# Kernel tuning notes

Measured on AMD Instinct MI355X. Metric: run time of the kernel, lower is better.

## Reference

```python
import jax, jax.numpy as jnp
import numpy as np

B, T, H, E = 256, 256, 512, 96  # batch, enc seq len, hidden/enc dim, charset size


def setup_inputs() -> dict:
    key = jax.random.key(0)
    ks = jax.random.split(key, 9)
    s = 0.05  # param scale
    return {
        "prev_h": jax.random.normal(ks[0], (B, H), jnp.float32),
        "prev_c": jax.random.normal(ks[1], (B, H), jnp.float32),
        "batch_H": jax.random.normal(ks[2], (B, T, H), jnp.float32),
        "char_onehots": jax.nn.one_hot(jax.random.randint(ks[3], (B,), 0, E), E, dtype=jnp.float32),
        "W_i2h": jax.random.normal(ks[4], (H, H), jnp.float32) * s,
        "W_h2h": jax.random.normal(ks[5], (H, H), jnp.float32) * s,
        "b_h2h": jnp.zeros((H,), jnp.float32),
        "w_score": jax.random.normal(ks[6], (H, 1), jnp.float32) * s,
        "W_lstm": jax.random.normal(ks[7], (H + E, 4 * H), jnp.float32) * s,
        "U_lstm": jax.random.normal(ks[8], (H, 4 * H), jnp.float32) * s,
        "b_lstm": jnp.zeros((4 * H,), jnp.float32),
    }


def reference(prev_h, prev_c, batch_H, char_onehots,
              W_i2h, W_h2h, b_h2h, w_score, W_lstm, U_lstm, b_lstm):
    # Additive (Bahdanau) attention
    proj = jnp.einsum('btd,dh->bth', batch_H, W_i2h)          # [B,T,H]
    hp = prev_h @ W_h2h + b_h2h                               # [B,H]
    e = jnp.tanh(proj + hp[:, None, :]) @ w_score             # [B,T,1]
    alpha = jax.nn.softmax(e, axis=1)                         # [B,T,1]
    context = jnp.einsum('bt,btd->bd', alpha[..., 0], batch_H)  # [B,D]
    x = jnp.concatenate([context, char_onehots], axis=1)      # [B,D+E]
    # Keras LSTMCell: gate order i, f, c(g), o
    z = x @ W_lstm + prev_h @ U_lstm + b_lstm                 # [B,4H]
    i, f, g, o = jnp.split(z, 4, axis=1)
    c_new = jax.nn.sigmoid(f) * prev_c + jax.nn.sigmoid(i) * jnp.tanh(g)
    h_new = jax.nn.sigmoid(o) * jnp.tanh(c_new)
    return h_new, c_new, alpha
```

## Files before the change

### kernel.cpp

```cpp
#include <hip/hip_runtime.h>
#include <hip/hip_bf16.h>
#include <math.h>

#define Bq 256
#define Tq 256
#define Hq 512
#define Eq 96

typedef __attribute__((ext_vector_type(8))) short short8;
typedef __attribute__((ext_vector_type(4))) float f32x4;

static __device__ __forceinline__ unsigned short f2bf(float f) {
  union { float f; unsigned u; } v; v.f = f;
  unsigned r = v.u + 0x7FFF + ((v.u >> 16) & 1);
  return (unsigned short)(r >> 16);
}

static __device__ __forceinline__ ushort4 pack4(float4 v) {
  ushort4 p;
  p.x = f2bf(v.x); p.y = f2bf(v.y); p.z = f2bf(v.z); p.w = f2bf(v.w);
  return p;
}

static __device__ __forceinline__ float sat_tanh(float x) {
  float ax = fminf(fabsf(x), 15.0f);
  float e = __builtin_exp2f(ax * 2.885390082f);
  float t = 1.0f - 2.0f / (e + 1.0f);
  return copysignf(t, x);
}

static __device__ __forceinline__ float sat_sig(float x) {
  float cx = fmaxf(fminf(x, 30.0f), -30.0f);
  return 1.0f / (1.0f + __builtin_exp2f(-cx * 1.442695041f));
}

__global__ __launch_bounds__(256) void convW_k(const float* __restrict__ W,
                                               unsigned short* __restrict__ Wt) {
  __shared__ float tile[32][33];
  int bx = blockIdx.x & 15, by = blockIdx.x >> 4;
  int tx = threadIdx.x & 31, ty = threadIdx.x >> 5;
  #pragma unroll
  for (int i = 0; i < 32; i += 8)
    tile[ty + i][tx] = W[(size_t)(by * 32 + ty + i) * Hq + bx * 32 + tx];
  __syncthreads();
  #pragma unroll
  for (int i = 0; i < 32; i += 8)
    Wt[(size_t)(bx * 32 + ty + i) * Hq + by * 32 + tx] = f2bf(tile[tx][ty + i]);
}

__global__ __launch_bounds__(256) void hsplit_k(const float* __restrict__ ph,
                                                const float* __restrict__ Whh,
                                                float* __restrict__ hp) {
  __shared__ __align__(16) float xs[8][128];
  const int ks = blockIdx.x & 3;
  const int nc = (blockIdx.x >> 2) & 3;
  const int bg = blockIdx.x >> 4;
  const int tid = threadIdx.x;
  const int row0 = bg * 8;
  const int d0 = ks * 128;
  for (int i = tid; i < 8 * 32; i += 256) {
    int r = i >> 5, dd = (i & 31) * 4;
    *(float4*)&xs[r][dd] = *(const float4*)&ph[(size_t)(row0 + r) * Hq + d0 + dd];
  }
  __syncthreads();
  const int rt = tid >> 6;
  const int ct = tid & 63;
  const int n = nc * 128 + ct * 2;
  float a00 = 0, a01 = 0, a10 = 0, a11 = 0;
  for (int dd = 0; dd < 128; dd += 4) {
    float4 x0 = *(const float4*)&xs[rt * 2][dd];
    float4 x1 = *(const float4*)&xs[rt * 2 + 1][dd];
    #pragma unroll
    for (int j = 0; j < 4; j++) {
      float2 w = *(const float2*)&Whh[(size_t)(d0 + dd + j) * Hq + n];
      float xj0 = ((const float*)&x0)[j];
      float xj1 = ((const float*)&x1)[j];
      a00 += xj0 * w.x; a01 += xj0 * w.y;
      a10 += xj1 * w.x; a11 += xj1 * w.y;
    }
  }
  int row = row0 + rt * 2;
  atomicAdd(&hp[(size_t)row * Hq + n], a00);
  atomicAdd(&hp[(size_t)row * Hq + n + 1], a01);
  atomicAdd(&hp[(size_t)(row + 1) * Hq + n], a10);
  atomicAdd(&hp[(size_t)(row + 1) * Hq + n + 1], a11);
}

#define LDK 40

__global__ __launch_bounds__(256, 2) void fused_score_k(
    const float* __restrict__ A,
    const unsigned short* __restrict__ Wt,
    const float* __restrict__ hp,
    const float* __restrict__ bh,
    const float* __restrict__ wsc,
    float* __restrict__ e) {
  __shared__ unsigned short As[2][64 * LDK];
  __shared__ float red[4][64];

  const int tid = threadIdx.x;
  const int m0 = blockIdx.x * 64;
  const int b = m0 >> 8;
  const int wave = tid >> 6;
  const int lane = tid & 63;
  const int quad = lane >> 4;
  const int l16 = lane & 15;
  const int wn = wave * 128;

  const int arow = tid >> 3;
  const int acol = (tid & 7) * 4;
  const float* Ab = A + (size_t)m0 * Hq;
  const unsigned short* Bp = Wt + (size_t)(wn + l16) * Hq + quad * 8;

  f32x4 acc[4][8] = {};

  {
    float4 v0 = *(const float4*)&Ab[(size_t)arow * Hq + acol];
    float4 v1 = *(const float4*)&Ab[(size_t)(arow + 32) * Hq + acol];
    *(ushort4*)&As[0][arow * LDK + acol] = pack4(v0);
    *(ushort4*)&As[0][(arow + 32) * LDK + acol] = pack4(v1);
  }
  __syncthreads();

  for (int step = 0; step < 16; step++) {
    const int k0 = step * 32;
    const int cur = step & 1;

    float4 n0v, n1v;
    if (step < 15) {
      n0v = *(const float4*)&Ab[(size_t)arow * Hq + k0 + 32 + acol];
      n1v = *(const float4*)&Ab[(size_t)(arow + 32) * Hq + k0 + 32 + acol];
    }

    short8 bfr[8];
    #pragma unroll
    for (int ni = 0; ni < 8; ni++)
      bfr[ni] = *(const short8*)(Bp + (size_t)ni * 16 * Hq + k0);

    short8 af[4];
    #pragma unroll
    for (int mi = 0; mi < 4; mi++)
      af[mi] = *(const short8*)&As[cur][(mi * 16 + l16) * LDK + quad * 8];

    #pragma unroll
    for (int mi = 0; mi < 4; mi++)
      #pragma unroll
      for (int ni = 0; ni < 8; ni++)
        acc[mi][ni] = __builtin_amdgcn_mfma_f32_16x16x32_bf16(
            af[mi], bfr[ni], acc[mi][ni], 0, 0, 0);

    if (step < 15) {
      *(ushort4*)&As[cur ^ 1][arow * LDK + acol] = pack4(n0v);
      *(ushort4*)&As[cur ^ 1][(arow + 32) * LDK + acol] = pack4(n1v);
    }
    __syncthreads();
  }

  float hv[8], wv[8];
  #pragma unroll
  for (int ni = 0; ni < 8; ni++) {
    int c = wn + ni * 16 + l16;
    hv[ni] = hp[(size_t)b * Hq + c] + bh[c];
    wv[ni] = wsc[c];
  }
  #pragma unroll
  for (int mi = 0; mi < 4; mi++) {
    float s[4] = {0, 0, 0, 0};
    #pragma unroll
    for (int ni = 0; ni < 8; ni++)
      #pragma unroll
      for (int r = 0; r < 4; r++)
        s[r] += sat_tanh(acc[mi][ni][r] + hv[ni]) * wv[ni];
    #pragma unroll
    for (int r = 0; r < 4; r++) {
      s[r] += __shfl_xor(s[r], 8, 64);
      s[r] += __shfl_xor(s[r], 4, 64);
      s[r] += __shfl_xor(s[r], 2, 64);
      s[r] += __shfl_xor(s[r], 1, 64);
    }
    if (l16 == 0) {
      #pragma unroll
      for (int r = 0; r < 4; r++) red[wave][mi * 16 + quad * 4 + r] = s[r];
    }
  }
  __syncthreads();
  if (tid < 64)
    e[m0 + tid] = red[0][tid] + red[1][tid] + red[2][tid] + red[3][tid];
}

__global__ __launch_bounds__(256) void softmax_k(float* __restrict__ ea) {
  __shared__ float red[8];
  int b = blockIdx.x, t = threadIdx.x;
  int wave = t >> 6, lane = t & 63;
  float x = ea[b * Tq + t];
  float m = x;
  #pragma unroll
  for (int off = 32; off >= 1; off >>= 1) m = fmaxf(m, __shfl_xor(m, off, 64));
  if (lane == 0) red[wave] = m;
  __syncthreads();
  m = fmaxf(fmaxf(red[0], red[1]), fmaxf(red[2], red[3]));
  float ex = __builtin_exp2f((x - m) * 1.442695041f);
  float s = ex;
  #pragma unroll
  for (int off = 32; off >= 1; off >>= 1) s += __shfl_xor(s, off, 64);
  if (lane == 0) red[4 + wave] = s;
  __syncthreads();
  s = red[4] + red[5] + red[6] + red[7];
  ea[b * Tq + t] = ex / s;
}

__global__ __launch_bounds__(256) void ctxsplit_k(const float* __restrict__ alpha,
                                                  const float* __restrict__ bH,
                                                  float* __restrict__ ctx) {
  __shared__ float al[64];
  const int b = blockIdx.x >> 2;
  const int tc = blockIdx.x & 3;
  const int tid = threadIdx.x;
  if (tid < 64) al[tid] = alpha[b * Tq + tc * 64 + tid];
  __syncthreads();
  const float2* Hp = (const float2*)(bH + (size_t)b * Tq * Hq + (size_t)tc * 64 * Hq);
  float ax = 0.f, ay = 0.f;
  #pragma unroll 8
  for (int t = 0; t < 64; t++) {
    float a = al[t];
    float2 v = Hp[t * (Hq / 2) + tid];
    ax += a * v.x;
    ay += a * v.y;
  }
  atomicAdd(&ctx[(size_t)b * Hq + 2 * tid], ax);
  atomicAdd(&ctx[(size_t)b * Hq + 2 * tid + 1], ay);
}

__global__ __launch_bounds__(256) void zsplit_k(
    const float* __restrict__ ctx, const float* __restrict__ oneh,
    const float* __restrict__ ph, const float* __restrict__ Wl,
    const float* __restrict__ Ul, float* __restrict__ z) {
  __shared__ __align__(16) float xs[8 * 280];
  const int ks = blockIdx.x & 3;
  const int hc = (blockIdx.x >> 2) & 7;
  const int bg = blockIdx.x >> 5;
  const int tid = threadIdx.x;
  const int row0 = bg * 8;
  const int dbase = ks * 280;

  for (int i = tid; i < 8 * 280; i += 256) {
    int r = i / 280, dd = i % 280;
    int g = dbase + dd;
    float v;
    if (g < 512) v = ctx[(size_t)(row0 + r) * Hq + g];
    else if (g < 608) v = oneh[(row0 + r) * Eq + (g - 512)];
    else v = ph[(size_t)(row0 + r) * Hq + (g - 608)];
    xs[r * 280 + dd] = v;
  }
  __syncthreads();

  const int rt = tid >> 6;
  const int ct = tid & 63;
  const int c0 = ct * 4;
  const int gate = c0 >> 6;
  const int ho = c0 & 63;
  const int n = gate * 512 + hc * 64 + ho;

  float acc0[4] = {0, 0, 0, 0};
  float acc1[4] = {0, 0, 0, 0};
  const float* xr0 = &xs[(rt * 2) * 280];
  const float* xr1 = &xs[(rt * 2 + 1) * 280];

  for (int dd = 0; dd < 280; dd += 4) {
    float4 x0 = *(const float4*)&xr0[dd];
    float4 x1 = *(const float4*)&xr1[dd];
    #pragma unroll
    for (int j = 0; j < 4; j++) {
      int d = dbase + dd + j;
      const float* wp = (d < 608) ? &Wl[(size_t)d * 2048 + n]
                                  : &Ul[(size_t)(d - 608) * 2048 + n];
      float4 w = *(const float4*)wp;
      float a = ((const float*)&x0)[j], b = ((const float*)&x1)[j];
      acc0[0] += a * w.x; acc0[1] += a * w.y; acc0[2] += a * w.z; acc0[3] += a * w.w;
      acc1[0] += b * w.x; acc1[1] += b * w.y; acc1[2] += b * w.z; acc1[3] += b * w.w;
    }
  }
  const int r0 = row0 + rt * 2;
  #pragma unroll
  for (int j = 0; j < 4; j++) {
    atomicAdd(&z[(size_t)r0 * 2048 + n + j], acc0[j]);
    atomicAdd(&z[(size_t)(r0 + 1) * 2048 + n + j], acc1[j]);
  }
}

__global__ __launch_bounds__(256) void gatesz_k(const float* __restrict__ z,
                                                const float* __restrict__ bl,
                                                const float* __restrict__ pc,
                                                float* __restrict__ outh,
                                                float* __restrict__ outc) {
  int p = blockIdx.x * 256 + threadIdx.x;
  #pragma unroll
  for (int q = 0; q < 2; q++, p += 65536) {
    int r = p >> 9, h = p & 511;
    const float* zb = z + (size_t)r * 2048;
    float gi = zb[h] + bl[h];
    float gf = zb[512 + h] + bl[512 + h];
    float gg = zb[1024 + h] + bl[1024 + h];
    float go = zb[1536 + h] + bl[1536 + h];
    float cn = sat_sig(gf) * pc[p] + sat_sig(gi) * sat_tanh(gg);
    float hn = sat_sig(go) * sat_tanh(cn);
    outh[p] = hn;
    outc[p] = cn;
  }
}

#define KXc 1120
__global__ __launch_bounds__(256) void zgates2_k(
    const float* __restrict__ ctx, const float* __restrict__ oneh,
    const float* __restrict__ ph, const float* __restrict__ pc,
    const float* __restrict__ Wl, const float* __restrict__ Ul,
    const float* __restrict__ bl,
    float* __restrict__ outh, float* __restrict__ outc) {
  __shared__ __align__(16) float xs[8 * KXc];
  const int bg = blockIdx.x >> 3;
  const int hc = blockIdx.x & 7;
  const int tid = threadIdx.x;
  const int row0 = bg * 8;

  for (int i = tid; i < 8 * 128; i += 256) {
    int r = i >> 7, dd = (i & 127) * 4;
    *(float4*)&xs[r * KXc + dd] = *(const float4*)&ctx[(size_t)(row0 + r) * Hq + dd];
  }
  for (int i = tid; i < 8 * 128; i += 256) {
    int r = i >> 7, dd = (i & 127) * 4;
    *(float4*)&xs[r * KXc + 608 + dd] = *(const float4*)&ph[(size_t)(row0 + r) * Hq + dd];
  }
  if (tid < 8 * 24) {
    int r = tid / 24, dd = (tid % 24) * 4;
    *(float4*)&xs[r * KXc + 512 + dd] = *(const float4*)&oneh[(row0 + r) * Eq + dd];
  }
  __syncthreads();

  const int rt = tid >> 6;
  const int ct = tid & 63;
  const int c0 = ct * 4;
  const int gate = c0 >> 6;
  const int ho = c0 & 63;
  const int n = gate * 512 + hc * 64 + ho;

  float acc0[4] = {0, 0, 0, 0};
  float acc1[4] = {0, 0, 0, 0};
  const float* xr0 = &xs[(rt * 2) * KXc];
  const float* xr1 = &xs[(rt * 2 + 1) * KXc];

  for (int d = 0; d < 608; d += 4) {
    float4 x0 = *(const float4*)&xr0[d];
    float4 x1 = *(const float4*)&xr1[d];
    #pragma unroll
    for (int j = 0; j < 4; j++) {
      float4 w = *(const float4*)&Wl[(size_t)(d + j) * 2048 + n];
      float a = ((const float*)&x0)[j], b = ((const float*)&x1)[j];
      acc0[0] += a * w.x; acc0[1] += a * w.y; acc0[2] += a * w.z; acc0[3] += a * w.w;
      acc1[0] += b * w.x; acc1[1] += b * w.y; acc1[2] += b * w.z; acc1[3] += b * w.w;
    }
  }
  for (int d = 0; d < 512; d += 4) {
    float4 x0 = *(const float4*)&xr0[608 + d];
    float4 x1 = *(const float4*)&xr1[608 + d];
    #pragma unroll
    for (int j = 0; j < 4; j++) {
      float4 w = *(const float4*)&Ul[(size_t)(d + j) * 2048 + n];
      float a = ((const float*)&x0)[j], b = ((const float*)&x1)[j];
      acc0[0] += a * w.x; acc0[1] += a * w.y; acc0[2] += a * w.z; acc0[3] += a * w.w;
      acc1[0] += b * w.x; acc1[1] += b * w.y; acc1[2] += b * w.z; acc1[3] += b * w.w;
    }
  }

  __syncthreads();
  float* zs = xs;
  #pragma unroll
  for (int j = 0; j < 4; j++) {
    zs[(rt * 2) * 256 + c0 + j] = acc0[j];
    zs[(rt * 2 + 1) * 256 + c0 + j] = acc1[j];
  }
  __syncthreads();

  #pragma unroll
  for (int p = tid; p < 512; p += 256) {
    int r = p >> 6, o = p & 63;
    int h = hc * 64 + o;
    int grow = row0 + r;
    float gi = zs[r * 256 + o]       + bl[h];
    float gf = zs[r * 256 + 64 + o]  + bl[512 + h];
    float gg = zs[r * 256 + 128 + o] + bl[1024 + h];
    float go = zs[r * 256 + 192 + o] + bl[1536 + h];
    float cn = sat_sig(gf) * pc[(size_t)grow * Hq + h] + sat_sig(gi) * sat_tanh(gg);
    float hn = sat_sig(go) * sat_tanh(cn);
    outh[(size_t)grow * Hq + h] = hn;
    outc[(size_t)grow * Hq + h] = cn;
  }
}

extern "C" void kernel_launch(void* const* d_in, const int* in_sizes, int n_in,
                              void* d_out, int out_size, void* d_ws, size_t ws_size,
                              hipStream_t stream) {
  const float* prev_h = (const float*)d_in[0];
  const float* prev_c = (const float*)d_in[1];
  const float* batch_H = (const float*)d_in[2];
  const float* oneh = (const float*)d_in[3];
  const float* W_i2h = (const float*)d_in[4];
  const float* W_h2h = (const float*)d_in[5];
  const float* b_h2h = (const float*)d_in[6];
  const float* w_score = (const float*)d_in[7];
  const float* W_lstm = (const float*)d_in[8];
  const float* U_lstm = (const float*)d_in[9];
  const float* b_lstm = (const float*)d_in[10];

  float* out = (float*)d_out;
  float* outh = out;
  float* outc = out + Bq * Hq;
  float* alpha = out + 2 * Bq * Hq;

  float* ws = (float*)d_ws;
  float* hp = ws;
  float* ctx = ws;
  unsigned short* Wt = (unsigned short*)(ws + 131072);
  float* z = ws + 131072;

  const bool bigws = ws_size >= 2621440;

  hipMemsetAsync(hp, 0, Bq * Hq * sizeof(float), stream);
  convW_k<<<256, 256, 0, stream>>>(W_i2h, Wt);
  hsplit_k<<<512, 256, 0, stream>>>(prev_h, W_h2h, hp);
  fused_score_k<<<1024, 256, 0, stream>>>(batch_H, Wt, hp, b_h2h, w_score, alpha);
  softmax_k<<<256, 256, 0, stream>>>(alpha);
  if (bigws) {
    hipMemsetAsync(ws, 0, 2621440, stream);
    ctxsplit_k<<<1024, 256, 0, stream>>>(alpha, batch_H, ctx);
    zsplit_k<<<1024, 256, 0, stream>>>(ctx, oneh, prev_h, W_lstm, U_lstm, z);
    gatesz_k<<<256, 256, 0, stream>>>(z, b_lstm, prev_c, outh, outc);
  } else {
    hipMemsetAsync(ctx, 0, Bq * Hq * sizeof(float), stream);
    ctxsplit_k<<<1024, 256, 0, stream>>>(alpha, batch_H, ctx);
    zgates2_k<<<256, 256, 0, stream>>>(ctx, oneh, prev_h, prev_c,
                                       W_lstm, U_lstm, b_lstm, outh, outc);
  }
}
```

Baseline: 399.2 us.

## Pre-convert batch_H to bf16 and use direct global-to-LDS loads in score GEMM

Measured after the change: 433.8 us. 1.09x slower.

```diff
diff --git a/kernel.cpp b/kernel.cpp
--- a/kernel.cpp
+++ b/kernel.cpp
@@ -32,6 +32,28 @@
 static __device__ __forceinline__ float sat_sig(float x) {
   float cx = fmaxf(fminf(x, 30.0f), -30.0f);
   return 1.0f / (1.0f + __builtin_exp2f(-cx * 1.442695041f));
+}
+
+static __device__ __forceinline__ void gload_lds16(const void* g, void* l) {
+  __builtin_amdgcn_global_load_lds(
+      (const __attribute__((address_space(1))) unsigned int*)g,
+      (__attribute__((address_space(3))) unsigned int*)l,
+      16, 0, 0);
+}
+
+__global__ __launch_bounds__(256) void convA_k(const float* __restrict__ A,
+                                               unsigned short* __restrict__ A2) {
+  size_t i = ((size_t)blockIdx.x * 256 + threadIdx.x) * 8;
+  const size_t stride = (size_t)2048 * 256 * 8;
+  #pragma unroll
+  for (int it = 0; it < 8; it++, i += stride) {
+    float4 v0 = *(const float4*)&A[i];
+    float4 v1 = *(const float4*)&A[i + 4];
+    ushort4 p0 = pack4(v0);
+    ushort4 p1 = pack4(v1);
+    *(ushort4*)&A2[i] = p0;
+    *(ushort4*)&A2[i + 4] = p1;
+  }
 }
 
 __global__ __launch_bounds__(256) void convW_k(const float* __restrict__ W,
@@ -86,8 +108,96 @@
   atomicAdd(&hp[(size_t)(row + 1) * Hq + n + 1], a11);
 }
 
+__global__ __launch_bounds__(512) void fused_score2_k(
+    const unsigned short* __restrict__ A2,
+    const unsigned short* __restrict__ Wt,
+    const float* __restrict__ hp,
+    const float* __restrict__ bh,
+    const float* __restrict__ wsc,
+    float* __restrict__ e) {
+  __shared__ unsigned short As[64 * 32];
+  __shared__ unsigned short Bs[512 * 32];
+  __shared__ float red[8][64];
+
+  const int tid = threadIdx.x;
+  const int m0 = blockIdx.x * 64;
+  const int b = m0 >> 8;
+  const int wave = tid >> 6;
+  const int lane = tid & 63;
+  const int quad = lane >> 4;
+  const int l16 = lane & 15;
+  const int wn = wave * 64;
+
+  const unsigned short* agp =
+      A2 + (size_t)(m0 + (tid >> 2)) * Hq + (tid & 3) * 8;
+  const unsigned short* bgp =
+      Wt + (size_t)(tid >> 2) * Hq + (tid & 3) * 8;
+  unsigned short* alds = As + wave * 512;
+  unsigned short* blds = Bs + wave * 512;
+
+  f32x4 acc[4][4] = {};
+
+  for (int k0 = 0; k0 < Hq; k0 += 32) {
+    __syncthreads();
+    if (wave < 4) gload_lds16(agp + k0, alds);
+    #pragma unroll
+    for (int c = 0; c < 4; c++)
+      gload_lds16(bgp + (size_t)c * 128 * Hq + k0, blds + c * 4096);
+    __syncthreads();
+
+    short8 af[4], bf[4];
+    #pragma unroll
+    for (int mi = 0; mi < 4; mi++)
+      af[mi] = *(const short8*)&As[(mi * 16 + l16) * 32 + quad * 8];
+    #pragma unroll
+    for (int ni = 0; ni < 4; ni++)
+      bf[ni] = *(const short8*)&Bs[(wn + ni * 16 + l16) * 32 + quad * 8];
+
+    #pragma unroll
+    for (int mi = 0; mi < 4; mi++)
+      #pragma unroll
+      for (int ni = 0; ni < 4; ni++)
+        acc[mi][ni] = __builtin_amdgcn_mfma_f32_16x16x32_bf16(
+            af[mi], bf[ni], acc[mi][ni], 0, 0, 0);
+  }
+
+  float hv[4], wv[4];
+  #pragma unroll
+  for (int ni = 0; ni < 4; ni++) {
+    int c = wn + ni * 16 + l16;
+    hv[ni] = hp[(size_t)b * Hq + c] + bh[c];
+    wv[ni] = wsc[c];
+  }
+  #pragma unroll
+  for (int mi = 0; mi < 4; mi++) {
+    float s[4] = {0, 0, 0, 0};
+    #pragma unroll
+    for (int ni = 0; ni < 4; ni++)
+      #pragma unroll
+      for (int r = 0; r < 4; r++)
+        s[r] += sat_tanh(acc[mi][ni][r] + hv[ni]) * wv[ni];
+    #pragma unroll
+    for (int r = 0; r < 4; r++) {
+      s[r] += __shfl_xor(s[r], 8, 64);
+      s[r] += __shfl_xor(s[r], 4, 64);
+      s[r] += __shfl_xor(s[r], 2, 64);
+      s[r] += __shfl_xor(s[r], 1, 64);
+    }
+    if (l16 == 0) {
+      #pragma unroll
+      for (int r = 0; r < 4; r++) red[wave][mi * 16 + quad * 4 + r] = s[r];
+    }
+  }
+  __syncthreads();
+  if (tid < 64) {
+    float t = 0.f;
+    #pragma unroll
+    for (int w = 0; w < 8; w++) t += red[w][tid];
+    e[m0 + tid] = t;
+  }
+}
+
 #define LDK 40
-
 __global__ __launch_bounds__(256, 2) void fused_score_k(
     const float* __restrict__ A,
     const unsigned short* __restrict__ Wt,
@@ -421,13 +531,20 @@
   float* ctx = ws;
   unsigned short* Wt = (unsigned short*)(ws + 131072);
   float* z = ws + 131072;
+  unsigned short* A2 = (unsigned short*)((char*)d_ws + 2621440);
 
   const bool bigws = ws_size >= 2621440;
+  const bool hugews = ws_size >= 2621440 + 67108864ull;
 
   hipMemsetAsync(hp, 0, Bq * Hq * sizeof(float), stream);
+  if (hugews) convA_k<<<2048, 256, 0, stream>>>(batch_H, A2);
   convW_k<<<256, 256, 0, stream>>>(W_i2h, Wt);
   hsplit_k<<<512, 256, 0, stream>>>(prev_h, W_h2h, hp);
-  fused_score_k<<<1024, 256, 0, stream>>>(batch_H, Wt, hp, b_h2h, w_score, alpha);
+  if (hugews) {
+    fused_score2_k<<<1024, 512, 0, stream>>>(A2, Wt, hp, b_h2h, w_score, alpha);
+  } else {
+    fused_score_k<<<1024, 256, 0, stream>>>(batch_H, Wt, hp, b_h2h, w_score, alpha);
+  }
   softmax_k<<<256, 256, 0, stream>>>(alpha);
   if (bigws) {
     hipMemsetAsync(ws, 0, 2621440, stream);
```

## Stage full-K A tile in LDS and split score GEMM over eight waves

Applied to the files above, without the earlier changes.

Measured after the change: 403.1 us. No clear change (+1.0%).

```diff
diff --git a/kernel.cpp b/kernel.cpp
--- a/kernel.cpp
+++ b/kernel.cpp
@@ -86,17 +86,17 @@
   atomicAdd(&hp[(size_t)(row + 1) * Hq + n + 1], a11);
 }
 
-#define LDK 40
-
-__global__ __launch_bounds__(256, 2) void fused_score_k(
+#define LDKA 520
+
+__global__ __launch_bounds__(512, 2) void fused_score3_k(
     const float* __restrict__ A,
     const unsigned short* __restrict__ Wt,
     const float* __restrict__ hp,
     const float* __restrict__ bh,
     const float* __restrict__ wsc,
     float* __restrict__ e) {
-  __shared__ unsigned short As[2][64 * LDK];
-  __shared__ float red[4][64];
+  __shared__ unsigned short As[64 * LDKA];
+  __shared__ float red[8][64];
 
   const int tid = threadIdx.x;
   const int m0 = blockIdx.x * 64;
@@ -105,60 +105,47 @@
   const int lane = tid & 63;
   const int quad = lane >> 4;
   const int l16 = lane & 15;
-  const int wn = wave * 128;
-
-  const int arow = tid >> 3;
-  const int acol = (tid & 7) * 4;
-  const float* Ab = A + (size_t)m0 * Hq;
+  const int wn = wave * 64;
+
+  {
+    const int sr = tid >> 3;
+    const int sc = (tid & 7) * 64;
+    const float* Ar = A + (size_t)(m0 + sr) * Hq + sc;
+    unsigned short* dst = &As[sr * LDKA + sc];
+    #pragma unroll
+    for (int j = 0; j < 64; j += 8) {
+      float4 v0 = *(const float4*)&Ar[j];
+      float4 v1 = *(const float4*)&Ar[j + 4];
+      *(ushort4*)&dst[j] = pack4(v0);
+      *(ushort4*)&dst[j + 4] = pack4(v1);
+    }
+  }
+  __syncthreads();
+
+  f32x4 acc[4][4] = {};
   const unsigned short* Bp = Wt + (size_t)(wn + l16) * Hq + quad * 8;
-
-  f32x4 acc[4][8] = {};
-
-  {
-    float4 v0 = *(const float4*)&Ab[(size_t)arow * Hq + acol];
-    float4 v1 = *(const float4*)&Ab[(size_t)(arow + 32) * Hq + acol];
-    *(ushort4*)&As[0][arow * LDK + acol] = pack4(v0);
-    *(ushort4*)&As[0][(arow + 32) * LDK + acol] = pack4(v1);
-  }
-  __syncthreads();
-
-  for (int step = 0; step < 16; step++) {
-    const int k0 = step * 32;
-    const int cur = step & 1;
-
-    float4 n0v, n1v;
-    if (step < 15) {
-      n0v = *(const float4*)&Ab[(size_t)arow * Hq + k0 + 32 + acol];
-      n1v = *(const float4*)&Ab[(size_t)(arow + 32) * Hq + k0 + 32 + acol];
-    }
-
-    short8 bfr[8];
-    #pragma unroll
-    for (int ni = 0; ni < 8; ni++)
-      bfr[ni] = *(const short8*)(Bp + (size_t)ni * 16 * Hq + k0);
-
+  const unsigned short* Ap = &As[l16 * LDKA + quad * 8];
+
+  #pragma unroll 4
+  for (int ks = 0; ks < 16; ks++) {
+    const int k0 = ks * 32;
     short8 af[4];
     #pragma unroll
     for (int mi = 0; mi < 4; mi++)
-      af[mi] = *(const short8*)&As[cur][(mi * 16 + l16) * LDK + quad * 8];
-
-    #pragma unroll
-    for (int mi = 0; mi < 4; mi++)
+      af[mi] = *(const short8*)(Ap + mi * 16 * LDKA + k0);
+    #pragma unroll
+    for (int ni = 0; ni < 4; ni++) {
+      short8 bf = *(const short8*)(Bp + (size_t)ni * 16 * Hq + k0);
       #pragma unroll
-      for (int ni = 0; ni < 8; ni++)
+      for (int mi = 0; mi < 4; mi++)
         acc[mi][ni] = __builtin_amdgcn_mfma_f32_16x16x32_bf16(
-            af[mi], bfr[ni], acc[mi][ni], 0, 0, 0);
-
-    if (step < 15) {
-      *(ushort4*)&As[cur ^ 1][arow * LDK + acol] = pack4(n0v);
-      *(ushort4*)&As[cur ^ 1][(arow + 32) * LDK + acol] = pack4(n1v);
-    }
-    __syncthreads();
-  }
-
-  float hv[8], wv[8];
-  #pragma unroll
-  for (int ni = 0; ni < 8; ni++) {
+            af[mi], bf, acc[mi][ni], 0, 0, 0);
+    }
+  }
+
+  float hv[4], wv[4];
+  #pragma unroll
+  for (int ni = 0; ni < 4; ni++) {
     int c = wn + ni * 16 + l16;
     hv[ni] = hp[(size_t)b * Hq + c] + bh[c];
     wv[ni] = wsc[c];
@@ -167,7 +154,7 @@
   for (int mi = 0; mi < 4; mi++) {
     float s[4] = {0, 0, 0, 0};
     #pragma unroll
-    for (int ni = 0; ni < 8; ni++)
+    for (int ni = 0; ni < 4; ni++)
       #pragma unroll
       for (int r = 0; r < 4; r++)
         s[r] += sat_tanh(acc[mi][ni][r] + hv[ni]) * wv[ni];
@@ -184,8 +171,12 @@
     }
   }
   __syncthreads();
-  if (tid < 64)
-    e[m0 + tid] = red[0][tid] + red[1][tid] + red[2][tid] + red[3][tid];
+  if (tid < 64) {
+    float t = 0.f;
+    #pragma unroll
+    for (int w = 0; w < 8; w++) t += red[w][tid];
+    e[m0 + tid] = t;
+  }
 }
 
 __global__ __launch_bounds__(256) void softmax_k(float* __restrict__ ea) {
@@ -427,7 +418,7 @@
   hipMemsetAsync(hp, 0, Bq * Hq * sizeof(float), stream);
   convW_k<<<256, 256, 0, stream>>>(W_i2h, Wt);
   hsplit_k<<<512, 256, 0, stream>>>(prev_h, W_h2h, hp);
-  fused_score_k<<<1024, 256, 0, stream>>>(batch_H, Wt, hp, b_h2h, w_score, alpha);
+  fused_score3_k<<<1024, 512, 0, stream>>>(batch_H, Wt, hp, b_h2h, w_score, alpha);
   softmax_k<<<256, 256, 0, stream>>>(alpha);
   if (bigws) {
     hipMemsetAsync(ws, 0, 2621440, stream);
```
